# Kernel optimization log

Measured on AMD Instinct MI355X. Metric: run time of the kernel, lower is better.

The kernel has to match this reference:

```python
import jax, jax.numpy as jnp
import numpy as np

DIM, HEADS, WIN = 256, 8, 8
HD = DIM // HEADS
SCALE = HD ** -0.5


def _rel_index(w):
    # Swin-style relative position index, computed statically in numpy
    coords = np.stack(np.meshgrid(np.arange(w), np.arange(w), indexing='ij'))  # (2,w,w)
    cf = coords.reshape(2, -1)                      # (2, w*w)
    rel = (cf[:, :, None] - cf[:, None, :]).transpose(1, 2, 0)  # (w*w, w*w, 2)
    rel = rel.copy()
    rel[:, :, 0] += w - 1
    rel[:, :, 1] += w - 1
    rel[:, :, 0] *= 2 * w - 1
    return rel.sum(-1)                              # (w*w, w*w)

REL_IDX = _rel_index(WIN)


def setup_inputs() -> dict:
    key = jax.random.key(0)
    ks = jax.random.split(key, 6)
    B, C, D, H, W = 8, DIM, 100, WIN, WIN
    return {
        'x': jax.random.normal(ks[0], (B, C, D, H, W), jnp.float32),
        'dwconv_w': jax.random.normal(ks[1], (C, C, 1, 3, 3), jnp.float32) * 0.02,
        'dwconv_b': jnp.zeros((C,), jnp.float32),
        'qkv_w': jax.random.normal(ks[2], (3 * C, C), jnp.float32) * 0.02,
        'qkv_b': jnp.zeros((3 * C,), jnp.float32),
        'proj_w': jax.random.normal(ks[3], (C, C), jnp.float32) * 0.02,
        'proj_b': jnp.zeros((C,), jnp.float32),
        'rpb_table': jax.random.normal(ks[4], ((2 * WIN - 1) ** 2, HEADS), jnp.float32) * 0.02,
    }


def reference(x, dwconv_w, dwconv_b, qkv_w, qkv_b, proj_w, proj_b, rpb_table):
    B, C, D, H, W = x.shape
    N = H * W
    # 'dwconv': full Conv3d, kernel (1,3,3), padding (0,1,1)
    xl = jax.lax.conv_general_dilated(
        x, dwconv_w, window_strides=(1, 1, 1),
        padding=[(0, 0), (1, 1), (1, 1)],
        dimension_numbers=('NCDHW', 'OIDHW', 'NCDHW'),
    ) + dwconv_b[None, :, None, None, None]
    # qkv: 1x1x1 conv == pointwise linear over channels
    qkv = jnp.einsum('oc,bcdhw->bodhw', qkv_w, xl) + qkv_b[None, :, None, None, None]
    # channel dim layout: (three, head, head_dim)
    qkv = qkv.reshape(B, 3, HEADS, HD, D, N)
    q, k, v = qkv[:, 0], qkv[:, 1], qkv[:, 2]      # each (B, HEADS, HD, D, N)
    attn = jnp.einsum('bhcdn,bhcdm->bdhnm', q * SCALE, k)  # (B, D, HEADS, N, N)
    bias = rpb_table[REL_IDX.reshape(-1)].reshape(N, N, HEADS).transpose(2, 0, 1)
    attn = jax.nn.softmax(attn + bias[None, None], axis=-1)
    xa = jnp.einsum('bdhnm,bhcdm->bhcdn', attn, v)  # (B, HEADS, HD, D, N)
    xa = xa.reshape(B, C, D, H, W)                  # channel = (head, head_dim)
    out = jnp.einsum('oc,bcdhw->bodhw', proj_w, xa) + proj_b[None, :, None, None, None]
    return out
```

## Files before the change

### kernel.cpp

```cpp
#include <hip/hip_runtime.h>
#include <cstdint>
#include <cstddef>

#define SCALEQ 0.17677669529663689f

typedef _Float16 half_t;
typedef _Float16 half8   __attribute__((ext_vector_type(8)));
typedef _Float16 half4v  __attribute__((ext_vector_type(4)));
typedef float    float4v __attribute__((ext_vector_type(4)));

#define GLDS16(gp, lp)                                                        \
  __builtin_amdgcn_global_load_lds(                                           \
      (const __attribute__((address_space(1))) void*)(gp),                    \
      (__attribute__((address_space(3))) void*)(lp), 16, 0, 0)

__global__ __launch_bounds__(256) void prep_all(
    const float* __restrict__ x, const float* __restrict__ dwconv_w,
    const float* __restrict__ qkv_w, const float* __restrict__ proj_w,
    const float* __restrict__ rpb, half_t* __restrict__ xpad,
    half_t* __restrict__ Wt, half_t* __restrict__ qw16,
    half_t* __restrict__ pw16, float* __restrict__ btab) {
  __shared__ float tile[128 * 65];
  const int blk = blockIdx.x, t = threadIdx.x;
  if (blk < 800) {
    const int bd = blk, b = bd / 100, d = bd % 100;
    for (int hf = 0; hf < 2; ++hf) {
      for (int i = 0; i < 32; ++i) {
        int idx = i * 256 + t, c = idx >> 6, hw = idx & 63;
        tile[c * 65 + hw] = x[(size_t)((b * 256 + hf * 128 + c) * 100 + d) * 64 + hw];
      }
      __syncthreads();
      for (int i = 0; i < 50; ++i) {
        int idx = i * 256 + t, cell = idx >> 7, c = idx & 127;
        int hh = cell / 10, ww = cell % 10;
        float v = 0.f;
        if (hh >= 1 && hh <= 8 && ww >= 1 && ww <= 8)
          v = tile[c * 65 + (hh - 1) * 8 + (ww - 1)];
        xpad[(size_t)(bd * 100 + cell) * 256 + hf * 128 + c] = (half_t)v;
      }
      __syncthreads();
    }
  } else if (blk < 944) {
    const int base = (blk - 800) * 4096;
#pragma unroll
    for (int i = 0; i < 16; ++i) {
      int idx = base + i * 256 + t;
      int tap = idx >> 16, rem = idx & 65535;
      int o = rem >> 8, c = rem & 255;
      Wt[idx] = (half_t)dwconv_w[(o * 256 + c) * 9 + tap];
    }
  } else if (blk < 1040) {
    const int base = (blk - 944) * 2048;
#pragma unroll
    for (int i = 0; i < 8; ++i) {
      int idx = base + i * 256 + t;
      float v = qkv_w[idx];
      if (idx < 65536) v *= SCALEQ;
      qw16[idx] = (half_t)v;
    }
  } else if (blk < 1072) {
    const int base = (blk - 1040) * 2048;
#pragma unroll
    for (int i = 0; i < 8; ++i) {
      int idx = base + i * 256 + t;
      pw16[idx] = (half_t)proj_w[idx];
    }
  } else {
    const int base = (blk - 1072) * 2048;
#pragma unroll
    for (int i = 0; i < 8; ++i) {
      int idx = base + i * 256 + t;
      int hd = idx >> 12, n = (idx >> 6) & 63, m = idx & 63;
      int h1 = n >> 3, w1 = n & 7, h2 = m >> 3, w2 = m & 7;
      int ridx = (h1 - h2 + 7) * 15 + (w1 - w2 + 7);
      btab[idx] = rpb[ridx * 8 + hd];
    }
  }
}

__global__ __launch_bounds__(256) void conv_kernel(
    const half_t* __restrict__ Wt, const half_t* __restrict__ xpad,
    const float* __restrict__ convb, half_t* __restrict__ xl) {
  __shared__ __align__(16) half_t Asm[128 * 64];
  __shared__ __align__(16) half_t Bsm[128 * 64];
  const int blk = blockIdx.x;
  const int o0 = (blk & 1) * 128;
  const int n0 = (blk >> 1) * 128;
  const int tid = threadIdx.x;
  const int wave = tid >> 6, lane = tid & 63;
  const int l15 = lane & 15, quad = lane >> 4;
  const int wm = wave >> 1, wn = wave & 1;
  const int srow = tid >> 3;
  const int cg = (tid & 7) ^ (srow & 7);

  int pixbase[4], arow[4];
#pragma unroll
  for (int i = 0; i < 4; ++i) {
    int P = n0 + srow + i * 32;
    int bd = P >> 6, hw = P & 63;
    pixbase[i] = (bd * 100 + (hw >> 3) * 10 + (hw & 7)) * 512 + cg * 16;
    arow[i] = (o0 + srow + i * 32) * 512 + cg * 16;
  }

  float4v acc[4][4];
#pragma unroll
  for (int mi = 0; mi < 4; ++mi)
#pragma unroll
    for (int ni = 0; ni < 4; ++ni) {
      float4v z = {0.f, 0.f, 0.f, 0.f};
      acc[mi][ni] = z;
    }

  const char* xpc = (const char*)xpad;
  for (int tap = 0; tap < 9; ++tap) {
    const char* wt = (const char*)Wt + tap * 131072;
    const int toff = ((tap / 3) * 10 + (tap % 3)) * 512;
    for (int c0 = 0; c0 < 512; c0 += 128) {
#pragma unroll
      for (int i = 0; i < 4; ++i) {
        GLDS16(wt + arow[i] + c0, (char*)Asm + i * 4096 + wave * 1024);
        GLDS16(xpc + pixbase[i] + toff + c0, (char*)Bsm + i * 4096 + wave * 1024);
      }
      __syncthreads();
#pragma unroll
      for (int kh = 0; kh < 2; ++kh) {
        half8 af[4], bf[4];
#pragma unroll
        for (int mi = 0; mi < 4; ++mi) {
          int r = wm * 64 + mi * 16 + l15;
          af[mi] = *(const half8*)&Asm[r * 64 + (((kh * 4 + quad) ^ (r & 7)) * 8)];
        }
#pragma unroll
        for (int ni = 0; ni < 4; ++ni) {
          int r = wn * 64 + ni * 16 + l15;
          bf[ni] = *(const half8*)&Bsm[r * 64 + (((kh * 4 + quad) ^ (r & 7)) * 8)];
        }
#pragma unroll
        for (int mi = 0; mi < 4; ++mi)
#pragma unroll
          for (int ni = 0; ni < 4; ++ni)
            acc[mi][ni] = __builtin_amdgcn_mfma_f32_16x16x32_f16(
                af[mi], bf[ni], acc[mi][ni], 0, 0, 0);
      }
      __syncthreads();
    }
  }
#pragma unroll
  for (int mi = 0; mi < 4; ++mi) {
    const int o4 = o0 + wm * 64 + mi * 16 + quad * 4;
    const float b0 = convb[o4], b1 = convb[o4 + 1], b2 = convb[o4 + 2], b3 = convb[o4 + 3];
#pragma unroll
    for (int ni = 0; ni < 4; ++ni) {
      const int P = n0 + wn * 64 + ni * 16 + l15;
      half4v h;
      h.x = (half_t)(acc[mi][ni].x + b0);
      h.y = (half_t)(acc[mi][ni].y + b1);
      h.z = (half_t)(acc[mi][ni].z + b2);
      h.w = (half_t)(acc[mi][ni].w + b3);
      *(half4v*)(xl + (size_t)P * 256 + o4) = h;
    }
  }
}

__global__ __launch_bounds__(512) void fused_tail4(
    const half_t* __restrict__ xlg, const half_t* __restrict__ qw,
    const float* __restrict__ qkvb, const float* __restrict__ btab,
    const half_t* __restrict__ pw, const float* __restrict__ projb,
    float* __restrict__ out32) {
  __shared__ __align__(16) half_t LS[78336];
  const int bd = blockIdx.x;
  const int tid = threadIdx.x;
  const int wave = tid >> 6, lane = tid & 63;
  const int l15 = lane & 15, quad = lane >> 4;
  const int head = wave;

  half_t* xlp = LS;
  half_t* xa = LS;
  float* T = (float*)LS;
  half_t* scr = LS + 16896 + wave * 7680;
  half_t* qsc = scr;
  half_t* ksc = scr + 2560;
  half_t* vsc = scr + 5120;
  half_t* Psc = scr;

  const half_t* Wq0 = qw + head * 32 * 256;
  const half_t* Wk0 = qw + 65536 + head * 32 * 256;
  const half_t* Wv0 = qw + 131072 + head * 32 * 256;

  half8 wq[8][2];
#pragma unroll
  for (int kh = 0; kh < 8; ++kh)
#pragma unroll
    for (int mi = 0; mi < 2; ++mi)
      wq[kh][mi] = *(const half8*)(Wq0 + (mi * 16 + l15) * 256 + kh * 32 + quad * 8);

  {
    const char* src = (const char*)(xlg + (size_t)bd * 64 * 256);
#pragma unroll
    for (int i = 0; i < 4; ++i) {
      int row = i * 16 + wave * 2 + (lane >> 5);
      int sch = (lane & 31) ^ (row & 7);
      GLDS16(src + row * 512 + sch * 16, (char*)xlp + (i * 16 + wave * 2) * 512);
    }
  }
  __syncthreads();

  half8 wk[8][2];
  {
    float4v acc[2][4];
#pragma unroll
    for (int mi = 0; mi < 2; ++mi)
#pragma unroll
      for (int ni = 0; ni < 4; ++ni) {
        float4v z = {0.f, 0.f, 0.f, 0.f};
        acc[mi][ni] = z;
      }
#pragma unroll
    for (int kh = 0; kh < 8; ++kh) {
      half8 bf[4];
#pragma unroll
      for (int ni = 0; ni < 4; ++ni) {
        int r = ni * 16 + l15;
        bf[ni] = *(const half8*)&xlp[r * 256 + (((kh * 4 + quad) ^ (r & 7)) * 8)];
      }
#pragma unroll
      for (int mi = 0; mi < 2; ++mi)
        wk[kh][mi] = *(const half8*)(Wk0 + (mi * 16 + l15) * 256 + kh * 32 + quad * 8);
#pragma unroll
      for (int mi = 0; mi < 2; ++mi)
#pragma unroll
        for (int ni = 0; ni < 4; ++ni)
          acc[mi][ni] = __builtin_amdgcn_mfma_f32_16x16x32_f16(
              wq[kh][mi], bf[ni], acc[mi][ni], 0, 0, 0);
    }
#pragma unroll
    for (int mi = 0; mi < 2; ++mi) {
      const float4v b4 = *(const float4v*)&qkvb[head * 32 + mi * 16 + quad * 4];
#pragma unroll
      for (int ni = 0; ni < 4; ++ni) {
        half4v h;
        h.x = (half_t)(acc[mi][ni].x + b4.x * SCALEQ);
        h.y = (half_t)(acc[mi][ni].y + b4.y * SCALEQ);
        h.z = (half_t)(acc[mi][ni].z + b4.z * SCALEQ);
        h.w = (half_t)(acc[mi][ni].w + b4.w * SCALEQ);
        *(half4v*)(qsc + (ni * 16 + l15) * 40 + mi * 16 + quad * 4) = h;
      }
    }
  }

  half8 wv[8][2];
  {
    float4v acc[2][4];
#pragma unroll
    for (int mi = 0; mi < 2; ++mi)
#pragma unroll
      for (int ni = 0; ni < 4; ++ni) {
        float4v z = {0.f, 0.f, 0.f, 0.f};
        acc[mi][ni] = z;
      }
#pragma unroll
    for (int kh = 0; kh < 8; ++kh) {
      half8 bf[4];
#pragma unroll
      for (int ni = 0; ni < 4; ++ni) {
        int r = ni * 16 + l15;
        bf[ni] = *(const half8*)&xlp[r * 256 + (((kh * 4 + quad) ^ (r & 7)) * 8)];
      }
#pragma unroll
      for (int mi = 0; mi < 2; ++mi)
        wv[kh][mi] = *(const half8*)(Wv0 + (mi * 16 + l15) * 256 + kh * 32 + quad * 8);
#pragma unroll
      for (int mi = 0; mi < 2; ++mi)
#pragma unroll
        for (int ni = 0; ni < 4; ++ni)
          acc[mi][ni] = __builtin_amdgcn_mfma_f32_16x16x32_f16(
              wk[kh][mi], bf[ni], acc[mi][ni], 0, 0, 0);
    }
#pragma unroll
    for (int mi = 0; mi < 2; ++mi) {
      const float4v b4 = *(const float4v*)&qkvb[256 + head * 32 + mi * 16 + quad * 4];
#pragma unroll
      for (int ni = 0; ni < 4; ++ni) {
        half4v h;
        h.x = (half_t)(acc[mi][ni].x + b4.x);
        h.y = (half_t)(acc[mi][ni].y + b4.y);
        h.z = (half_t)(acc[mi][ni].z + b4.z);
        h.w = (half_t)(acc[mi][ni].w + b4.w);
        *(half4v*)(ksc + (ni * 16 + l15) * 40 + mi * 16 + quad * 4) = h;
      }
    }
  }

  {
    float4v acc[2][4];
#pragma unroll
    for (int mi = 0; mi < 2; ++mi)
#pragma unroll
      for (int ni = 0; ni < 4; ++ni) {
        float4v z = {0.f, 0.f, 0.f, 0.f};
        acc[mi][ni] = z;
      }
#pragma unroll
    for (int kh = 0; kh < 8; ++kh) {
      half8 bf[4];
#pragma unroll
      for (int ni = 0; ni < 4; ++ni) {
        int r = ni * 16 + l15;
        bf[ni] = *(const half8*)&xlp[r * 256 + (((kh * 4 + quad) ^ (r & 7)) * 8)];
      }
#pragma unroll
      for (int mi = 0; mi < 2; ++mi)
#pragma unroll
        for (int ni = 0; ni < 4; ++ni)
          acc[mi][ni] = __builtin_amdgcn_mfma_f32_16x16x32_f16(
              wv[kh][mi], bf[ni], acc[mi][ni], 0, 0, 0);
    }
#pragma unroll
    for (int mi = 0; mi < 2; ++mi) {
      const float4v b4 = *(const float4v*)&qkvb[512 + head * 32 + mi * 16 + quad * 4];
#pragma unroll
      for (int ni = 0; ni < 4; ++ni) {
#pragma unroll
        for (int iv = 0; iv < 4; ++iv)
          vsc[(mi * 16 + quad * 4 + iv) * 72 + ni * 16 + l15] =
              (half_t)(acc[mi][ni][iv] + b4[iv]);
      }
    }
  }

  __builtin_amdgcn_s_waitcnt(0);

  half8 aq[4], bk[4];
#pragma unroll
  for (int i = 0; i < 4; ++i) {
    aq[i] = *(const half8*)(qsc + (i * 16 + l15) * 40 + quad * 8);
    bk[i] = *(const half8*)(ksc + (i * 16 + l15) * 40 + quad * 8);
  }
  const float* bh = btab + head * 4096;
  float br[4][4][4];
#pragma unroll
  for (int ni = 0; ni < 4; ++ni)
#pragma unroll
    for (int i = 0; i < 4; ++i) {
      const int n = ni * 16 + quad * 4 + i;
#pragma unroll
      for (int mi = 0; mi < 4; ++mi)
        br[ni][i][mi] = bh[n * 64 + mi * 16 + l15];
    }
  float4v s[4][4];
#pragma unroll
  for (int ni = 0; ni < 4; ++ni)
#pragma unroll
    for (int mi = 0; mi < 4; ++mi) {
      float4v z = {0.f, 0.f, 0.f, 0.f};
      s[ni][mi] = __builtin_amdgcn_mfma_f32_16x16x32_f16(aq[ni], bk[mi], z, 0, 0, 0);
    }
#pragma unroll
  for (int ni = 0; ni < 4; ++ni)
#pragma unroll
    for (int i = 0; i < 4; ++i)
#pragma unroll
      for (int mi = 0; mi < 4; ++mi) s[ni][mi][i] += br[ni][i][mi];
  float inv[4][4];
#pragma unroll
  for (int ni = 0; ni < 4; ++ni)
#pragma unroll
    for (int i = 0; i < 4; ++i) {
      float mx = fmaxf(fmaxf(s[ni][0][i], s[ni][1][i]), fmaxf(s[ni][2][i], s[ni][3][i]));
      for (int off = 1; off < 16; off <<= 1) mx = fmaxf(mx, __shfl_xor(mx, off));
      float sum = 0.f;
#pragma unroll
      for (int mi = 0; mi < 4; ++mi) {
        float e = __expf(s[ni][mi][i] - mx);
        s[ni][mi][i] = e;
        sum += e;
      }
      for (int off = 1; off < 16; off <<= 1) sum += __shfl_xor(sum, off);
      inv[ni][i] = 1.0f / sum;
    }
#pragma unroll
  for (int ni = 0; ni < 4; ++ni)
#pragma unroll
    for (int i = 0; i < 4; ++i) {
      const int n = ni * 16 + quad * 4 + i;
#pragma unroll
      for (int mi = 0; mi < 4; ++mi)
        Psc[n * 72 + mi * 16 + l15] = (half_t)(s[ni][mi][i] * inv[ni][i]);
    }
  __builtin_amdgcn_s_waitcnt(0);

  half8 wp[8][2];
#pragma unroll
  for (int kh = 0; kh < 8; ++kh)
#pragma unroll
    for (int mi = 0; mi < 2; ++mi)
      wp[kh][mi] = *(const half8*)(pw + (wave * 32 + mi * 16 + l15) * 256 + kh * 32 + quad * 8);
  half8 av[2][2];
#pragma unroll
  for (int ci = 0; ci < 2; ++ci)
#pragma unroll
    for (int k2 = 0; k2 < 2; ++k2)
      av[ci][k2] = *(const half8*)(vsc + (ci * 16 + l15) * 72 + k2 * 32 + quad * 8);
  float4v oa[2][4];
#pragma unroll
  for (int ci = 0; ci < 2; ++ci)
#pragma unroll
    for (int ni = 0; ni < 4; ++ni) {
      float4v z = {0.f, 0.f, 0.f, 0.f};
      oa[ci][ni] = z;
    }
#pragma unroll
  for (int ni = 0; ni < 4; ++ni)
#pragma unroll
    for (int k2 = 0; k2 < 2; ++k2) {
      half8 bp = *(const half8*)&Psc[(ni * 16 + l15) * 72 + k2 * 32 + quad * 8];
#pragma unroll
      for (int ci = 0; ci < 2; ++ci)
        oa[ci][ni] = __builtin_amdgcn_mfma_f32_16x16x32_f16(av[ci][k2], bp, oa[ci][ni], 0, 0, 0);
    }

  __syncthreads();

#pragma unroll
  for (int ci = 0; ci < 2; ++ci)
#pragma unroll
    for (int ni = 0; ni < 4; ++ni) {
      half4v h = {(half_t)oa[ci][ni].x, (half_t)oa[ci][ni].y,
                  (half_t)oa[ci][ni].z, (half_t)oa[ci][ni].w};
      *(half4v*)(xa + (ni * 16 + l15) * 264 + head * 32 + ci * 16 + quad * 4) = h;
    }
  __syncthreads();

  float4v pacc[2][4];
#pragma unroll
  for (int mi = 0; mi < 2; ++mi)
#pragma unroll
    for (int ni = 0; ni < 4; ++ni) {
      float4v z = {0.f, 0.f, 0.f, 0.f};
      pacc[mi][ni] = z;
    }
#pragma unroll
  for (int kh = 0; kh < 8; ++kh) {
    half8 bf[4];
#pragma unroll
    for (int ni = 0; ni < 4; ++ni)
      bf[ni] = *(const half8*)&xa[(ni * 16 + l15) * 264 + kh * 32 + quad * 8];
#pragma unroll
    for (int mi = 0; mi < 2; ++mi)
#pragma unroll
      for (int ni = 0; ni < 4; ++ni)
        pacc[mi][ni] = __builtin_amdgcn_mfma_f32_16x16x32_f16(
            wp[kh][mi], bf[ni], pacc[mi][ni], 0, 0, 0);
  }
#pragma unroll
  for (int mi = 0; mi < 2; ++mi) {
    const float4v b4 = *(const float4v*)&projb[wave * 32 + mi * 16 + quad * 4];
#pragma unroll
    for (int ni = 0; ni < 4; ++ni) {
      pacc[mi][ni].x += b4.x;
      pacc[mi][ni].y += b4.y;
      pacc[mi][ni].z += b4.z;
      pacc[mi][ni].w += b4.w;
    }
  }

  const int b = bd / 100, d = bd % 100;
  const size_t bdbase = (size_t)b * 1638400 + (size_t)d * 64;
  const int tr = tid >> 3;
  const int col0 = (tid & 7) * 8;
  for (int r = 0; r < 4; ++r) {
    __syncthreads();
    if ((wave >> 1) == r) {
      const int rb = (wave & 1) * 32;
#pragma unroll
      for (int mi = 0; mi < 2; ++mi)
#pragma unroll
        for (int ni = 0; ni < 4; ++ni)
#pragma unroll
          for (int iv = 0; iv < 4; ++iv)
            T[(rb + mi * 16 + quad * 4 + iv) * 68 + ni * 16 + l15] = pacc[mi][ni][iv];
    }
    __syncthreads();
    const int o = r * 64 + tr;
    float* dst = out32 + bdbase + (size_t)o * 6400 + col0;
    const float* srcT = &T[tr * 68 + col0];
    *(float4v*)dst = *(const float4v*)srcT;
    *(float4v*)(dst + 4) = *(const float4v*)(srcT + 4);
  }
}

extern "C" void kernel_launch(void* const* d_in, const int* in_sizes, int n_in,
                              void* d_out, int out_size, void* d_ws, size_t ws_size,
                              hipStream_t stream) {
  const float* x        = (const float*)d_in[0];
  const float* dwconv_w = (const float*)d_in[1];
  const float* dwconv_b = (const float*)d_in[2];
  const float* qkv_w    = (const float*)d_in[3];
  const float* qkv_b    = (const float*)d_in[4];
  const float* proj_w   = (const float*)d_in[5];
  const float* proj_b   = (const float*)d_in[6];
  const float* rpb      = (const float*)d_in[7];
  float* out = (float*)d_out;

  char* ws = (char*)d_ws;
  size_t off = 0;
  half_t* xpad = (half_t*)(ws + off); off += 40960000;
  half_t* xl   = (half_t*)(ws + off); off += 26214400;
  half_t* Wt   = (half_t*)(ws + off); off += 1179648;
  half_t* qw16 = (half_t*)(ws + off); off += 393216;
  half_t* pw16 = (half_t*)(ws + off); off += 131072;
  float*  btab = (float*)(ws + off);  off += 131072;

  prep_all<<<1088, 256, 0, stream>>>(x, dwconv_w, qkv_w, proj_w, rpb,
                                     xpad, Wt, qw16, pw16, btab);
  conv_kernel<<<800, 256, 0, stream>>>(Wt, xpad, dwconv_b, xl);
  fused_tail4<<<800, 512, 0, stream>>>(xl, qw16, qkv_b, btab, pw16, proj_b, out);
}
```

Before: 292.1 us.

## Fuse 3x3 conv into attention tail kernel, keeping conv output in LDS

Removes the separate conv_kernel and computes the 3x3 conv for each (b,d) window inside the fused attention kernel. The padded input tile is staged into LDS and the conv output is written straight into the swizzled LDS buffer. That avoids the global write and re-read of the xl intermediate and one kernel launch. The conv weights are laid out again in prep so each wave can read its MFMA A-fragments directly from global memory, without LDS staging. The trade-offs are that each workgroup now computes only 64 pixels per conv, with weights re-read from global/L2 by every workgroup, and the conv reuse is lower than the old 128x128 tile GEMM.

```diff
diff --git a/kernel.cpp b/kernel.cpp
--- a/kernel.cpp
+++ b/kernel.cpp
@@ -45,8 +45,10 @@
 #pragma unroll
     for (int i = 0; i < 16; ++i) {
       int idx = base + i * 256 + t;
-      int tap = idx >> 16, rem = idx & 65535;
-      int o = rem >> 8, c = rem & 255;
+      int tap = idx >> 16;
+      int og = (idx >> 12) & 15, kh = (idx >> 9) & 7;
+      int l15o = (idx >> 5) & 15, c5 = idx & 31;
+      int o = og * 16 + l15o, c = kh * 32 + c5;
       Wt[idx] = (half_t)dwconv_w[(o * 256 + c) * 9 + tap];
     }
   } else if (blk < 1040) {
@@ -78,92 +80,9 @@
   }
 }
 
-__global__ __launch_bounds__(256) void conv_kernel(
-    const half_t* __restrict__ Wt, const half_t* __restrict__ xpad,
-    const float* __restrict__ convb, half_t* __restrict__ xl) {
-  __shared__ __align__(16) half_t Asm[128 * 64];
-  __shared__ __align__(16) half_t Bsm[128 * 64];
-  const int blk = blockIdx.x;
-  const int o0 = (blk & 1) * 128;
-  const int n0 = (blk >> 1) * 128;
-  const int tid = threadIdx.x;
-  const int wave = tid >> 6, lane = tid & 63;
-  const int l15 = lane & 15, quad = lane >> 4;
-  const int wm = wave >> 1, wn = wave & 1;
-  const int srow = tid >> 3;
-  const int cg = (tid & 7) ^ (srow & 7);
-
-  int pixbase[4], arow[4];
-#pragma unroll
-  for (int i = 0; i < 4; ++i) {
-    int P = n0 + srow + i * 32;
-    int bd = P >> 6, hw = P & 63;
-    pixbase[i] = (bd * 100 + (hw >> 3) * 10 + (hw & 7)) * 512 + cg * 16;
-    arow[i] = (o0 + srow + i * 32) * 512 + cg * 16;
-  }
-
-  float4v acc[4][4];
-#pragma unroll
-  for (int mi = 0; mi < 4; ++mi)
-#pragma unroll
-    for (int ni = 0; ni < 4; ++ni) {
-      float4v z = {0.f, 0.f, 0.f, 0.f};
-      acc[mi][ni] = z;
-    }
-
-  const char* xpc = (const char*)xpad;
-  for (int tap = 0; tap < 9; ++tap) {
-    const char* wt = (const char*)Wt + tap * 131072;
-    const int toff = ((tap / 3) * 10 + (tap % 3)) * 512;
-    for (int c0 = 0; c0 < 512; c0 += 128) {
-#pragma unroll
-      for (int i = 0; i < 4; ++i) {
-        GLDS16(wt + arow[i] + c0, (char*)Asm + i * 4096 + wave * 1024);
-        GLDS16(xpc + pixbase[i] + toff + c0, (char*)Bsm + i * 4096 + wave * 1024);
-      }
-      __syncthreads();
-#pragma unroll
-      for (int kh = 0; kh < 2; ++kh) {
-        half8 af[4], bf[4];
-#pragma unroll
-        for (int mi = 0; mi < 4; ++mi) {
-          int r = wm * 64 + mi * 16 + l15;
-          af[mi] = *(const half8*)&Asm[r * 64 + (((kh * 4 + quad) ^ (r & 7)) * 8)];
-        }
-#pragma unroll
-        for (int ni = 0; ni < 4; ++ni) {
-          int r = wn * 64 + ni * 16 + l15;
-          bf[ni] = *(const half8*)&Bsm[r * 64 + (((kh * 4 + quad) ^ (r & 7)) * 8)];
-        }
-#pragma unroll
-        for (int mi = 0; mi < 4; ++mi)
-#pragma unroll
-          for (int ni = 0; ni < 4; ++ni)
-            acc[mi][ni] = __builtin_amdgcn_mfma_f32_16x16x32_f16(
-                af[mi], bf[ni], acc[mi][ni], 0, 0, 0);
-      }
-      __syncthreads();
-    }
-  }
-#pragma unroll
-  for (int mi = 0; mi < 4; ++mi) {
-    const int o4 = o0 + wm * 64 + mi * 16 + quad * 4;
-    const float b0 = convb[o4], b1 = convb[o4 + 1], b2 = convb[o4 + 2], b3 = convb[o4 + 3];
-#pragma unroll
-    for (int ni = 0; ni < 4; ++ni) {
-      const int P = n0 + wn * 64 + ni * 16 + l15;
-      half4v h;
-      h.x = (half_t)(acc[mi][ni].x + b0);
-      h.y = (half_t)(acc[mi][ni].y + b1);
-      h.z = (half_t)(acc[mi][ni].z + b2);
-      h.w = (half_t)(acc[mi][ni].w + b3);
-      *(half4v*)(xl + (size_t)P * 256 + o4) = h;
-    }
-  }
-}
-
-__global__ __launch_bounds__(512) void fused_tail4(
-    const half_t* __restrict__ xlg, const half_t* __restrict__ qw,
+__global__ __launch_bounds__(512) void fused_all(
+    const half_t* __restrict__ xpg, const half_t* __restrict__ Wt,
+    const float* __restrict__ convb, const half_t* __restrict__ qw,
     const float* __restrict__ qkvb, const float* __restrict__ btab,
     const half_t* __restrict__ pw, const float* __restrict__ projb,
     float* __restrict__ out32) {
@@ -177,6 +96,7 @@
   half_t* xlp = LS;
   half_t* xa = LS;
   float* T = (float*)LS;
+  half_t* xpl = LS + 16896;
   half_t* scr = LS + 16896 + wave * 7680;
   half_t* qsc = scr;
   half_t* ksc = scr + 2560;
@@ -187,6 +107,74 @@
   const half_t* Wk0 = qw + 65536 + head * 32 * 256;
   const half_t* Wv0 = qw + 131072 + head * 32 * 256;
 
+  {
+    const char* src = (const char*)(xpg + (size_t)bd * 25600);
+    const int cid = wave * 64 + lane;
+#pragma unroll
+    for (int i = 0; i < 7; ++i) {
+      const int chunkid = i * 512 + cid;
+      if (chunkid < 3200) {
+        const int cell = chunkid >> 5, p = chunkid & 31;
+        const int g = (p & 24) | ((p ^ cell) & 7);
+        GLDS16(src + cell * 512 + g * 16,
+               (char*)xpl + (i * 512 + wave * 64) * 16);
+      }
+    }
+  }
+  __syncthreads();
+
+  {
+    const int pxb = (l15 >> 3) * 10 + (l15 & 7);
+    float4v acc[2][4];
+#pragma unroll
+    for (int mi = 0; mi < 2; ++mi)
+#pragma unroll
+      for (int ni = 0; ni < 4; ++ni) {
+        float4v z = {0.f, 0.f, 0.f, 0.f};
+        acc[mi][ni] = z;
+      }
+    const half_t* wv0 = Wt + (wave * 2) * 4096 + l15 * 32 + quad * 8;
+#pragma unroll 1
+    for (int tap = 0; tap < 9; ++tap) {
+      const int tc = (tap / 3) * 10 + (tap % 3);
+      const half_t* wt = wv0 + tap * 65536;
+      const int c0 = pxb + tc;
+#pragma unroll
+      for (int kh = 0; kh < 8; ++kh) {
+        half8 af0 = *(const half8*)(wt + kh * 512);
+        half8 af1 = *(const half8*)(wt + 4096 + kh * 512);
+        half8 bf[4];
+#pragma unroll
+        for (int ni = 0; ni < 4; ++ni) {
+          const int cell = c0 + ni * 20;
+          bf[ni] = *(const half8*)&xpl[cell * 256 + (((kh * 4 + quad) ^ (cell & 7)) * 8)];
+        }
+#pragma unroll
+        for (int ni = 0; ni < 4; ++ni) {
+          acc[0][ni] = __builtin_amdgcn_mfma_f32_16x16x32_f16(af0, bf[ni], acc[0][ni], 0, 0, 0);
+          acc[1][ni] = __builtin_amdgcn_mfma_f32_16x16x32_f16(af1, bf[ni], acc[1][ni], 0, 0, 0);
+        }
+      }
+    }
+#pragma unroll
+    for (int mi = 0; mi < 2; ++mi) {
+      const int o4 = wave * 32 + mi * 16 + quad * 4;
+      const float4v b4 = *(const float4v*)&convb[o4];
+      const int chunk = o4 >> 3;
+      const int sub = (quad & 1) * 4;
+#pragma unroll
+      for (int ni = 0; ni < 4; ++ni) {
+        const int px = ni * 16 + l15;
+        half4v h;
+        h.x = (half_t)(acc[mi][ni].x + b4.x);
+        h.y = (half_t)(acc[mi][ni].y + b4.y);
+        h.z = (half_t)(acc[mi][ni].z + b4.z);
+        h.w = (half_t)(acc[mi][ni].w + b4.w);
+        *(half4v*)&xlp[px * 256 + ((chunk ^ (px & 7)) * 8) + sub] = h;
+      }
+    }
+  }
+
   half8 wq[8][2];
 #pragma unroll
   for (int kh = 0; kh < 8; ++kh)
@@ -194,15 +182,6 @@
     for (int mi = 0; mi < 2; ++mi)
       wq[kh][mi] = *(const half8*)(Wq0 + (mi * 16 + l15) * 256 + kh * 32 + quad * 8);
 
-  {
-    const char* src = (const char*)(xlg + (size_t)bd * 64 * 256);
-#pragma unroll
-    for (int i = 0; i < 4; ++i) {
-      int row = i * 16 + wave * 2 + (lane >> 5);
-      int sch = (lane & 31) ^ (row & 7);
-      GLDS16(src + row * 512 + sch * 16, (char*)xlp + (i * 16 + wave * 2) * 512);
-    }
-  }
   __syncthreads();
 
   half8 wk[8][2];
@@ -505,7 +484,6 @@
   char* ws = (char*)d_ws;
   size_t off = 0;
   half_t* xpad = (half_t*)(ws + off); off += 40960000;
-  half_t* xl   = (half_t*)(ws + off); off += 26214400;
   half_t* Wt   = (half_t*)(ws + off); off += 1179648;
   half_t* qw16 = (half_t*)(ws + off); off += 393216;
   half_t* pw16 = (half_t*)(ws + off); off += 131072;
@@ -513,6 +491,6 @@
 
   prep_all<<<1088, 256, 0, stream>>>(x, dwconv_w, qkv_w, proj_w, rpb,
                                      xpad, Wt, qw16, pw16, btab);
-  conv_kernel<<<800, 256, 0, stream>>>(Wt, xpad, dwconv_b, xl);
-  fused_tail4<<<800, 512, 0, stream>>>(xl, qw16, qkv_b, btab, pw16, proj_b, out);
+  fused_all<<<800, 512, 0, stream>>>(xpad, Wt, dwconv_b, qw16, qkv_b, btab,
+                                     pw16, proj_b, out);
 }
```

After: 310.2 us. +6.2%, slower.
